# Kernel tuning notes

Measured on AMD Instinct MI355X. Metric: run time of the kernel, lower is better.

## Reference

```python
import jax, jax.numpy as jnp
import numpy as np

N_NODES = 50000
N_EDGES = 800000
D = 128
D_OUT = 128


def setup_inputs() -> dict:
    key = jax.random.key(0)
    k1, k2, k3, k4, k5 = jax.random.split(key, 5)
    feature = jax.random.normal(k1, (N_NODES, D), dtype=jnp.float32)
    src = jax.random.randint(k2, (N_EDGES,), 0, N_NODES)
    dst = jax.random.randint(k3, (N_EDGES,), 0, N_NODES)
    W = jax.random.normal(k4, (D_OUT, 2 * D), dtype=jnp.float32) * (1.0 / np.sqrt(2 * D))
    b = jax.random.normal(k5, (D_OUT,), dtype=jnp.float32) * 0.01
    return {"feature": feature, "src": src, "dst": dst, "W": W, "b": b}


def reference(feature, src, dst, W, b):
    # copy_src: message m_e = feature[src_e]; mean reduce over incoming edges per dst node
    msgs = feature[src]                                             # [E, D] gather
    agg = jax.ops.segment_sum(msgs, dst, num_segments=N_NODES)      # [N, D]
    deg = jax.ops.segment_sum(jnp.ones((N_EDGES,), jnp.float32), dst,
                              num_segments=N_NODES)                 # [N]
    h = agg / jnp.maximum(deg, 1.0)[:, None]                        # mean; 0-degree nodes stay 0
    x = jnp.concatenate([h, feature], axis=1)                       # [N, 2D]
    return x @ W.T + b                                              # [N, D_OUT]
```

## Files before the change

### kernel.cpp

```cpp
#include <hip/hip_runtime.h>
#include <hip/hip_bf16.h>


#define D_IN 128
#define NB 391
#define BSHIFT 7
#define EPB 4096
#define CAPMAX 2680

typedef __attribute__((ext_vector_type(8))) short bf16x8;
typedef __attribute__((ext_vector_type(4))) float f32x4;

static __device__ inline unsigned short f2bf(float x) {
    union { float f; unsigned u; } c; c.f = x;
    unsigned u = c.u;
    unsigned r = u + 0x7FFFu + ((u >> 16) & 1u);
    return (unsigned short)(r >> 16);
}
static __device__ inline float bflo(unsigned u) { return __uint_as_float(u << 16); }
static __device__ inline float bfhi(unsigned u) { return __uint_as_float(u & 0xFFFF0000u); }

__global__ __launch_bounds__(256) void convert_kernel(const float* __restrict__ feat,
                                                      const float* __restrict__ W,
                                                      unsigned short* __restrict__ X,
                                                      unsigned short* __restrict__ Wbf,
                                                      int* __restrict__ bcursor,
                                                      int M, int blocks_f, int CAP) {
    int b = blockIdx.x;
    if (b < blocks_f) {
        size_t idx = ((size_t)b * 256 + threadIdx.x) * 8;
        if (idx >= (size_t)M * 128) return;
        int row = (int)(idx >> 7);
        int col = (int)(idx & 127);
        float4 v0 = *reinterpret_cast<const float4*>(feat + idx);
        float4 v1 = *reinterpret_cast<const float4*>(feat + idx + 4);
        uint4 p;
        p.x = (unsigned)f2bf(v0.x) | ((unsigned)f2bf(v0.y) << 16);
        p.y = (unsigned)f2bf(v0.z) | ((unsigned)f2bf(v0.w) << 16);
        p.z = (unsigned)f2bf(v1.x) | ((unsigned)f2bf(v1.y) << 16);
        p.w = (unsigned)f2bf(v1.z) | ((unsigned)f2bf(v1.w) << 16);
        *reinterpret_cast<uint4*>(X + (size_t)row * 256 + 128 + col) = p;
    } else if (b < blocks_f + 16) {
        int idx = ((b - blocks_f) * 256 + (int)threadIdx.x) * 8;
        if (idx >= 128 * 256) return;
        float4 v0 = *reinterpret_cast<const float4*>(W + idx);
        float4 v1 = *reinterpret_cast<const float4*>(W + idx + 4);
        uint4 p;
        p.x = (unsigned)f2bf(v0.x) | ((unsigned)f2bf(v0.y) << 16);
        p.y = (unsigned)f2bf(v0.z) | ((unsigned)f2bf(v0.w) << 16);
        p.z = (unsigned)f2bf(v1.x) | ((unsigned)f2bf(v1.y) << 16);
        p.w = (unsigned)f2bf(v1.z) | ((unsigned)f2bf(v1.w) << 16);
        *reinterpret_cast<uint4*>(Wbf + idx) = p;
    } else {
        for (int i = threadIdx.x; i < NB; i += 256) bcursor[i] = i * CAP;
    }
}

__global__ __launch_bounds__(256) void coarse_scatter_kernel(
    const int* __restrict__ src, const int* __restrict__ dst,
    int* __restrict__ bcursor, unsigned* __restrict__ bedges,
    int CAP, int nE) {
    __shared__ int hist[NB];
    __shared__ int lofs[NB + 1];
    __shared__ int rnk[NB];
    __shared__ int gbase[NB];
    __shared__ int wsum[4];
    __shared__ unsigned staged[EPB];

    const int tid = threadIdx.x;
    const int e0 = blockIdx.x * EPB;
    for (int i = tid; i < NB; i += 256) { hist[i] = 0; rnk[i] = 0; }
    __syncthreads();

    for (int k = 0; k < EPB; k += 256) {
        int e = e0 + k + tid;
        if (e < nE) atomicAdd(&hist[dst[e] >> BSHIFT], 1);
    }
    __syncthreads();

    {
        int a = (2 * tid < NB) ? hist[2 * tid] : 0;
        int c = (2 * tid + 1 < NB) ? hist[2 * tid + 1] : 0;
        int ps = a + c;
        int x = ps;
        int lane = tid & 63, wv = tid >> 6;
#pragma unroll
        for (int off = 1; off < 64; off <<= 1) {
            int y = __shfl_up(x, off);
            if (lane >= off) x += y;
        }
        if (lane == 63) wsum[wv] = x;
        __syncthreads();
        if (tid == 0) {
            int s = 0;
#pragma unroll
            for (int w = 0; w < 4; w++) { int v = wsum[w]; wsum[w] = s; s += v; }
        }
        __syncthreads();
        int excl = x - ps + wsum[wv];
        if (2 * tid < NB + 1) lofs[2 * tid] = excl;
        if (2 * tid + 1 < NB + 1) lofs[2 * tid + 1] = excl + a;
    }
    __syncthreads();

    for (int i = tid; i < NB; i += 256)
        if (hist[i] > 0) gbase[i] = atomicAdd(&bcursor[i], hist[i]);

    for (int k = 0; k < EPB; k += 256) {
        int e = e0 + k + tid;
        if (e < nE) {
            int d = dst[e];
            int bk = d >> BSHIFT;
            unsigned ed = ((unsigned)d << 16) | (unsigned)src[e];
            int r = atomicAdd(&rnk[bk], 1);
            staged[lofs[bk] + r] = ed;
        }
    }
    __syncthreads();

    int total = lofs[NB];
    for (int i = tid; i < total; i += 256) {
        unsigned ed = staged[i];
        int bk = (int)(ed >> 23);
        int addr = gbase[bk] + (i - lofs[bk]);
        if (addr < (bk + 1) * CAP) bedges[addr] = ed;
    }
}

__global__ __launch_bounds__(256) void fine_sort_kernel(
    unsigned* __restrict__ bedges, const int* __restrict__ bcursor,
    unsigned* __restrict__ rstart, int CAP, int N) {
    __shared__ int h[128];
    __shared__ int lofs[129];
    __shared__ int rnk[128];
    __shared__ unsigned staged[CAPMAX + 8];

    const int b = blockIdx.x;
    const int S = b * CAP;
    const int tid = threadIdx.x;
    int cnt = min(bcursor[b] - S, CAP);

    if (tid < 128) { h[tid] = 0; rnk[tid] = 0; }
    __syncthreads();
    for (int i = tid; i < cnt; i += 256) {
        unsigned ed = bedges[S + i];
        atomicAdd(&h[(ed >> 16) & 127], 1);
    }
    __syncthreads();
    if (tid < 64) {
        int a = h[2 * tid], c = h[2 * tid + 1];
        int ps = a + c;
        int x = ps;
#pragma unroll
        for (int off = 1; off < 64; off <<= 1) {
            int y = __shfl_up(x, off);
            if (tid >= off) x += y;
        }
        int excl = x - ps;
        lofs[2 * tid] = excl;
        lofs[2 * tid + 1] = excl + a;
        if (tid == 63) lofs[128] = x;
    }
    __syncthreads();
    for (int i = tid; i < cnt; i += 256) {
        unsigned ed = bedges[S + i];
        int ld = (ed >> 16) & 127;
        int r = atomicAdd(&rnk[ld], 1);
        staged[lofs[ld] + r] = ed;
    }
    __syncthreads();
    for (int i = tid; i < cnt; i += 256) bedges[S + i] = staged[i];
    if (tid < 128) {
        int node = b * 128 + tid;
        if (node < N)
            rstart[node] = (((unsigned)(S + lofs[tid])) << 12) | (unsigned)h[tid];
    }
}

__global__ __launch_bounds__(256) void node_agg_kernel(unsigned short* __restrict__ X,
                                                       const unsigned* __restrict__ bedges,
                                                       const unsigned* __restrict__ rstart, int N) {
    int wid = (int)((blockIdx.x * (size_t)blockDim.x + threadIdx.x) >> 6);
    if (wid >= N) return;
    const int lane = threadIdx.x & 63;
    const int q = lane >> 4;
    const int sl = lane & 15;
    const unsigned pk = rstart[wid];
    const int s = (int)(pk >> 12);
    const int cnt = (int)(pk & 4095u);
    const int e = s + cnt;
    const char* Xb = (const char*)X;
    const size_t coff = 256 + (size_t)sl * 16;

    float a0=0.f,a1=0.f,a2=0.f,a3=0.f,a4=0.f,a5=0.f,a6=0.f,a7=0.f;
    int j = s + q;
    for (; j + 4 < e; j += 8) {
        int u0 = (int)(bedges[j] & 0xFFFFu);
        int u1 = (int)(bedges[j + 4] & 0xFFFFu);
        uint4 va = *reinterpret_cast<const uint4*>(Xb + (size_t)u0 * 512 + coff);
        uint4 vb = *reinterpret_cast<const uint4*>(Xb + (size_t)u1 * 512 + coff);
        a0 += bflo(va.x) + bflo(vb.x); a1 += bfhi(va.x) + bfhi(vb.x);
        a2 += bflo(va.y) + bflo(vb.y); a3 += bfhi(va.y) + bfhi(vb.y);
        a4 += bflo(va.z) + bflo(vb.z); a5 += bfhi(va.z) + bfhi(vb.z);
        a6 += bflo(va.w) + bflo(vb.w); a7 += bfhi(va.w) + bfhi(vb.w);
    }
    if (j < e) {
        int u = (int)(bedges[j] & 0xFFFFu);
        uint4 va = *reinterpret_cast<const uint4*>(Xb + (size_t)u * 512 + coff);
        a0 += bflo(va.x); a1 += bfhi(va.x);
        a2 += bflo(va.y); a3 += bfhi(va.y);
        a4 += bflo(va.z); a5 += bfhi(va.z);
        a6 += bflo(va.w); a7 += bfhi(va.w);
    }
    a0 += __shfl_down(a0, 32); a1 += __shfl_down(a1, 32);
    a2 += __shfl_down(a2, 32); a3 += __shfl_down(a3, 32);
    a4 += __shfl_down(a4, 32); a5 += __shfl_down(a5, 32);
    a6 += __shfl_down(a6, 32); a7 += __shfl_down(a7, 32);
    a0 += __shfl_down(a0, 16); a1 += __shfl_down(a1, 16);
    a2 += __shfl_down(a2, 16); a3 += __shfl_down(a3, 16);
    a4 += __shfl_down(a4, 16); a5 += __shfl_down(a5, 16);
    a6 += __shfl_down(a6, 16); a7 += __shfl_down(a7, 16);
    if (lane < 16) {
        float r = 1.0f / fmaxf((float)cnt, 1.0f);
        uint4 p;
        p.x = (unsigned)f2bf(a0 * r) | ((unsigned)f2bf(a1 * r) << 16);
        p.y = (unsigned)f2bf(a2 * r) | ((unsigned)f2bf(a3 * r) << 16);
        p.z = (unsigned)f2bf(a4 * r) | ((unsigned)f2bf(a5 * r) << 16);
        p.w = (unsigned)f2bf(a6 * r) | ((unsigned)f2bf(a7 * r) << 16);
        *reinterpret_cast<uint4*>((char*)X + (size_t)wid * 512 + sl * 16) = p;
    }
}

__global__ __launch_bounds__(256) void gcn_gemm_kernel(
    const unsigned short* __restrict__ X, const unsigned short* __restrict__ Wbf,
    const float* __restrict__ bias, float* __restrict__ out, int M) {

    __shared__ unsigned short A_sh[128 * 128];
    __shared__ unsigned short B_sh[128 * 128];
    char* Ab = (char*)A_sh;
    char* Bb = (char*)B_sh;
    const char* Xb = (const char*)X;
    const char* Wb = (const char*)Wbf;

    const int tid = threadIdx.x;
    const int n0 = blockIdx.x * 128;
    const int wid = tid >> 6;
    const int lane = tid & 63;
    const int wr = wid >> 1;
    const int wc = wid & 1;
    const int fr = lane & 15;
    const int fq = lane >> 4;

    f32x4 acc[4][4];
#pragma unroll
    for (int m = 0; m < 4; m++)
#pragma unroll
        for (int n = 0; n < 4; n++) acc[m][n] = (f32x4)(0.0f);

#pragma unroll
    for (int p = 0; p < 2; p++) {
#pragma unroll
        for (int it = 0; it < 8; it++) {
            int idx = it * 256 + tid;
            int row = idx >> 4;
            int ch = idx & 15;
            int off = ((row << 8) + (ch << 4)) ^ ((row & 7) << 4);
            int nrow = n0 + row;
            uint4 va = make_uint4(0u, 0u, 0u, 0u);
            if (nrow < M)
                va = *reinterpret_cast<const uint4*>(Xb + (size_t)nrow * 512 + p * 256 + ch * 16);
            *reinterpret_cast<uint4*>(Ab + off) = va;
            uint4 vb = *reinterpret_cast<const uint4*>(Wb + (size_t)row * 512 + p * 256 + ch * 16);
            *reinterpret_cast<uint4*>(Bb + off) = vb;
        }
        __syncthreads();

#pragma unroll
        for (int ks = 0; ks < 4; ks++) {
            const int k = ks * 32 + fq * 8;
            bf16x8 af[4], bf_[4];
#pragma unroll
            for (int m = 0; m < 4; m++) {
                int row = wr * 64 + m * 16 + fr;
                int off = ((row << 8) + (k << 1)) ^ ((row & 7) << 4);
                af[m] = *reinterpret_cast<const bf16x8*>(Ab + off);
            }
#pragma unroll
            for (int n = 0; n < 4; n++) {
                int col = wc * 64 + n * 16 + fr;
                int off = ((col << 8) + (k << 1)) ^ ((col & 7) << 4);
                bf_[n] = *reinterpret_cast<const bf16x8*>(Bb + off);
            }
#pragma unroll
            for (int m = 0; m < 4; m++)
#pragma unroll
                for (int n = 0; n < 4; n++)
                    acc[m][n] = __builtin_amdgcn_mfma_f32_16x16x32_bf16(af[m], bf_[n], acc[m][n], 0, 0, 0);
        }
        if (p == 0) __syncthreads();
    }

    float bv[4];
#pragma unroll
    for (int n = 0; n < 4; n++) bv[n] = bias[wc * 64 + n * 16 + fr];

#pragma unroll
    for (int m = 0; m < 4; m++) {
        int rbase = n0 + wr * 64 + m * 16 + fq * 4;
#pragma unroll
        for (int n = 0; n < 4; n++) {
            int col = wc * 64 + n * 16 + fr;
#pragma unroll
            for (int j = 0; j < 4; j++) {
                int r = rbase + j;
                if (r < M) out[(size_t)r * 128 + col] = acc[m][n][j] + bv[n];
            }
        }
    }
}

extern "C" void kernel_launch(void* const* d_in, const int* in_sizes, int n_in,
                              void* d_out, int out_size, void* d_ws, size_t ws_size,
                              hipStream_t stream) {
    const float* feature = (const float*)d_in[0];
    const int*   src     = (const int*)d_in[1];
    const int*   dst     = (const int*)d_in[2];
    const float* W       = (const float*)d_in[3];
    const float* bias    = (const float*)d_in[4];
    float* out = (float*)d_out;

    const int M  = in_sizes[0] / D_IN;
    const int nE = in_sizes[1];

    char* w = (char*)d_ws;
    unsigned short* X   = (unsigned short*)w;
    unsigned short* Wbf = X + (size_t)M * 256;
    int* bcursor = (int*)(Wbf + 128 * 256);
    unsigned* rstart = (unsigned*)(bcursor + NB);
    unsigned* bedges = (unsigned*)(rstart + M);

    size_t fixed = (size_t)((char*)bedges - w);
    long avail = (long)ws_size - (long)fixed;
    int CAP = (int)(avail / (NB * 4));
    if (CAP > CAPMAX) CAP = CAPMAX;
    if (CAP < 1) CAP = 1;

    const int blocks_f = (M * D_IN) / (256 * 8);
    convert_kernel<<<blocks_f + 17, 256, 0, stream>>>(feature, W, X, Wbf, bcursor, M, blocks_f, CAP);
    {
        int blocks = (nE + EPB - 1) / EPB;
        coarse_scatter_kernel<<<blocks, 256, 0, stream>>>(src, dst, bcursor, bedges, CAP, nE);
    }
    {
        int blocks = (M + 127) / 128;
        fine_sort_kernel<<<blocks, 256, 0, stream>>>(bedges, bcursor, rstart, CAP, M);
    }
    {
        size_t totalT = (size_t)M * 64;
        int blocks = (int)((totalT + 255) / 256);
        node_agg_kernel<<<blocks, 256, 0, stream>>>(X, bedges, rstart, M);
    }
    {
        int blocks = (M + 127) / 128;
        gcn_gemm_kernel<<<blocks, 256, 0, stream>>>(X, Wbf, bias, out, M);
    }
}
```

Baseline: 79.87 us.

## Fuse convert with coarse scatter and fine sort with node aggregation

The feature/W conversion and the coarse edge bucketing now run as one kernel, with bucket cursors zeroed by a memset and stored as offsets relative to each bucket. The fine per-bucket sort and the mean aggregation are merged into one 512-thread kernel. It reads the sorted edges straight from LDS, so the sorted-edge write-back and the rstart array are gone. This removes two kernel launches and a global round trip of the edge list. In exchange, aggregation parallelism drops to 8 waves per 128-node bucket, and the gather loop is unrolled to 4 edges per lane.

```diff
diff --git a/kernel.cpp b/kernel.cpp
--- a/kernel.cpp
+++ b/kernel.cpp
@@ -20,15 +20,25 @@
 static __device__ inline float bflo(unsigned u) { return __uint_as_float(u << 16); }
 static __device__ inline float bfhi(unsigned u) { return __uint_as_float(u & 0xFFFF0000u); }
 
-__global__ __launch_bounds__(256) void convert_kernel(const float* __restrict__ feat,
-                                                      const float* __restrict__ W,
-                                                      unsigned short* __restrict__ X,
-                                                      unsigned short* __restrict__ Wbf,
-                                                      int* __restrict__ bcursor,
-                                                      int M, int blocks_f, int CAP) {
-    int b = blockIdx.x;
+__global__ __launch_bounds__(256) void prep_kernel(
+    const float* __restrict__ feat, const float* __restrict__ W,
+    const int* __restrict__ src, const int* __restrict__ dst,
+    unsigned short* __restrict__ X, unsigned short* __restrict__ Wbf,
+    int* __restrict__ bcursor, unsigned* __restrict__ bedges,
+    int M, int nE, int blocks_f, int CAP) {
+
+    __shared__ int hist[NB];
+    __shared__ int lofs[NB + 1];
+    __shared__ int rnk[NB];
+    __shared__ int gbase[NB];
+    __shared__ int wsum[4];
+    __shared__ unsigned staged[EPB];
+
+    const int b = blockIdx.x;
+    const int tid = threadIdx.x;
+
     if (b < blocks_f) {
-        size_t idx = ((size_t)b * 256 + threadIdx.x) * 8;
+        size_t idx = ((size_t)b * 256 + tid) * 8;
         if (idx >= (size_t)M * 128) return;
         int row = (int)(idx >> 7);
         int col = (int)(idx & 127);
@@ -40,8 +50,10 @@
         p.z = (unsigned)f2bf(v1.x) | ((unsigned)f2bf(v1.y) << 16);
         p.w = (unsigned)f2bf(v1.z) | ((unsigned)f2bf(v1.w) << 16);
         *reinterpret_cast<uint4*>(X + (size_t)row * 256 + 128 + col) = p;
-    } else if (b < blocks_f + 16) {
-        int idx = ((b - blocks_f) * 256 + (int)threadIdx.x) * 8;
+        return;
+    }
+    if (b < blocks_f + 16) {
+        int idx = ((b - blocks_f) * 256 + tid) * 8;
         if (idx >= 128 * 256) return;
         float4 v0 = *reinterpret_cast<const float4*>(W + idx);
         float4 v1 = *reinterpret_cast<const float4*>(W + idx + 4);
@@ -51,24 +63,10 @@
         p.z = (unsigned)f2bf(v1.x) | ((unsigned)f2bf(v1.y) << 16);
         p.w = (unsigned)f2bf(v1.z) | ((unsigned)f2bf(v1.w) << 16);
         *reinterpret_cast<uint4*>(Wbf + idx) = p;
-    } else {
-        for (int i = threadIdx.x; i < NB; i += 256) bcursor[i] = i * CAP;
-    }
-}
-
-__global__ __launch_bounds__(256) void coarse_scatter_kernel(
-    const int* __restrict__ src, const int* __restrict__ dst,
-    int* __restrict__ bcursor, unsigned* __restrict__ bedges,
-    int CAP, int nE) {
-    __shared__ int hist[NB];
-    __shared__ int lofs[NB + 1];
-    __shared__ int rnk[NB];
-    __shared__ int gbase[NB];
-    __shared__ int wsum[4];
-    __shared__ unsigned staged[EPB];
-
-    const int tid = threadIdx.x;
-    const int e0 = blockIdx.x * EPB;
+        return;
+    }
+
+    const int e0 = (b - blocks_f - 16) * EPB;
     for (int i = tid; i < NB; i += 256) { hist[i] = 0; rnk[i] = 0; }
     __syncthreads();
 
@@ -104,7 +102,7 @@
     __syncthreads();
 
     for (int i = tid; i < NB; i += 256)
-        if (hist[i] > 0) gbase[i] = atomicAdd(&bcursor[i], hist[i]);
+        if (hist[i] > 0) gbase[i] = i * CAP + atomicAdd(&bcursor[i], hist[i]);
 
     for (int k = 0; k < EPB; k += 256) {
         int e = e0 + k + tid;
@@ -127,9 +125,10 @@
     }
 }
 
-__global__ __launch_bounds__(256) void fine_sort_kernel(
-    unsigned* __restrict__ bedges, const int* __restrict__ bcursor,
-    unsigned* __restrict__ rstart, int CAP, int N) {
+__global__ __launch_bounds__(512) void sort_agg_kernel(
+    unsigned short* __restrict__ X, const unsigned* __restrict__ bedges,
+    const int* __restrict__ bcursor, int CAP, int N) {
+
     __shared__ int h[128];
     __shared__ int lofs[129];
     __shared__ int rnk[128];
@@ -138,11 +137,11 @@
     const int b = blockIdx.x;
     const int S = b * CAP;
     const int tid = threadIdx.x;
-    int cnt = min(bcursor[b] - S, CAP);
+    const int cnt = min(bcursor[b], CAP);
 
     if (tid < 128) { h[tid] = 0; rnk[tid] = 0; }
     __syncthreads();
-    for (int i = tid; i < cnt; i += 256) {
+    for (int i = tid; i < cnt; i += 512) {
         unsigned ed = bedges[S + i];
         atomicAdd(&h[(ed >> 16) & 127], 1);
     }
@@ -162,72 +161,74 @@
         if (tid == 63) lofs[128] = x;
     }
     __syncthreads();
-    for (int i = tid; i < cnt; i += 256) {
+    for (int i = tid; i < cnt; i += 512) {
         unsigned ed = bedges[S + i];
         int ld = (ed >> 16) & 127;
         int r = atomicAdd(&rnk[ld], 1);
         staged[lofs[ld] + r] = ed;
     }
     __syncthreads();
-    for (int i = tid; i < cnt; i += 256) bedges[S + i] = staged[i];
-    if (tid < 128) {
-        int node = b * 128 + tid;
-        if (node < N)
-            rstart[node] = (((unsigned)(S + lofs[tid])) << 12) | (unsigned)h[tid];
-    }
-}
-
-__global__ __launch_bounds__(256) void node_agg_kernel(unsigned short* __restrict__ X,
-                                                       const unsigned* __restrict__ bedges,
-                                                       const unsigned* __restrict__ rstart, int N) {
-    int wid = (int)((blockIdx.x * (size_t)blockDim.x + threadIdx.x) >> 6);
-    if (wid >= N) return;
-    const int lane = threadIdx.x & 63;
+
+    const int w = tid >> 6;
+    const int lane = tid & 63;
     const int q = lane >> 4;
     const int sl = lane & 15;
-    const unsigned pk = rstart[wid];
-    const int s = (int)(pk >> 12);
-    const int cnt = (int)(pk & 4095u);
-    const int e = s + cnt;
     const char* Xb = (const char*)X;
     const size_t coff = 256 + (size_t)sl * 16;
-
-    float a0=0.f,a1=0.f,a2=0.f,a3=0.f,a4=0.f,a5=0.f,a6=0.f,a7=0.f;
-    int j = s + q;
-    for (; j + 4 < e; j += 8) {
-        int u0 = (int)(bedges[j] & 0xFFFFu);
-        int u1 = (int)(bedges[j + 4] & 0xFFFFu);
-        uint4 va = *reinterpret_cast<const uint4*>(Xb + (size_t)u0 * 512 + coff);
-        uint4 vb = *reinterpret_cast<const uint4*>(Xb + (size_t)u1 * 512 + coff);
-        a0 += bflo(va.x) + bflo(vb.x); a1 += bfhi(va.x) + bfhi(vb.x);
-        a2 += bflo(va.y) + bflo(vb.y); a3 += bfhi(va.y) + bfhi(vb.y);
-        a4 += bflo(va.z) + bflo(vb.z); a5 += bfhi(va.z) + bfhi(vb.z);
-        a6 += bflo(va.w) + bflo(vb.w); a7 += bfhi(va.w) + bfhi(vb.w);
-    }
-    if (j < e) {
-        int u = (int)(bedges[j] & 0xFFFFu);
-        uint4 va = *reinterpret_cast<const uint4*>(Xb + (size_t)u * 512 + coff);
-        a0 += bflo(va.x); a1 += bfhi(va.x);
-        a2 += bflo(va.y); a3 += bfhi(va.y);
-        a4 += bflo(va.z); a5 += bfhi(va.z);
-        a6 += bflo(va.w); a7 += bfhi(va.w);
-    }
-    a0 += __shfl_down(a0, 32); a1 += __shfl_down(a1, 32);
-    a2 += __shfl_down(a2, 32); a3 += __shfl_down(a3, 32);
-    a4 += __shfl_down(a4, 32); a5 += __shfl_down(a5, 32);
-    a6 += __shfl_down(a6, 32); a7 += __shfl_down(a7, 32);
-    a0 += __shfl_down(a0, 16); a1 += __shfl_down(a1, 16);
-    a2 += __shfl_down(a2, 16); a3 += __shfl_down(a3, 16);
-    a4 += __shfl_down(a4, 16); a5 += __shfl_down(a5, 16);
-    a6 += __shfl_down(a6, 16); a7 += __shfl_down(a7, 16);
-    if (lane < 16) {
-        float r = 1.0f / fmaxf((float)cnt, 1.0f);
-        uint4 p;
-        p.x = (unsigned)f2bf(a0 * r) | ((unsigned)f2bf(a1 * r) << 16);
-        p.y = (unsigned)f2bf(a2 * r) | ((unsigned)f2bf(a3 * r) << 16);
-        p.z = (unsigned)f2bf(a4 * r) | ((unsigned)f2bf(a5 * r) << 16);
-        p.w = (unsigned)f2bf(a6 * r) | ((unsigned)f2bf(a7 * r) << 16);
-        *reinterpret_cast<uint4*>((char*)X + (size_t)wid * 512 + sl * 16) = p;
+    const int n0 = b * 128;
+
+    for (int ln = w; ln < 128; ln += 8) {
+        int node = n0 + ln;
+        if (node >= N) break;
+        const int s = lofs[ln];
+        const int deg = h[ln];
+        const int e = s + deg;
+
+        float a0=0.f,a1=0.f,a2=0.f,a3=0.f,a4=0.f,a5=0.f,a6=0.f,a7=0.f;
+        int j = s + q;
+        for (; j + 12 < e; j += 16) {
+            int u0 = (int)(staged[j] & 0xFFFFu);
+            int u1 = (int)(staged[j + 4] & 0xFFFFu);
+            int u2 = (int)(staged[j + 8] & 0xFFFFu);
+            int u3 = (int)(staged[j + 12] & 0xFFFFu);
+            uint4 va = *reinterpret_cast<const uint4*>(Xb + (size_t)u0 * 512 + coff);
+            uint4 vb = *reinterpret_cast<const uint4*>(Xb + (size_t)u1 * 512 + coff);
+            uint4 vc = *reinterpret_cast<const uint4*>(Xb + (size_t)u2 * 512 + coff);
+            uint4 vd = *reinterpret_cast<const uint4*>(Xb + (size_t)u3 * 512 + coff);
+            a0 += (bflo(va.x) + bflo(vb.x)) + (bflo(vc.x) + bflo(vd.x));
+            a1 += (bfhi(va.x) + bfhi(vb.x)) + (bfhi(vc.x) + bfhi(vd.x));
+            a2 += (bflo(va.y) + bflo(vb.y)) + (bflo(vc.y) + bflo(vd.y));
+            a3 += (bfhi(va.y) + bfhi(vb.y)) + (bfhi(vc.y) + bfhi(vd.y));
+            a4 += (bflo(va.z) + bflo(vb.z)) + (bflo(vc.z) + bflo(vd.z));
+            a5 += (bfhi(va.z) + bfhi(vb.z)) + (bfhi(vc.z) + bfhi(vd.z));
+            a6 += (bflo(va.w) + bflo(vb.w)) + (bflo(vc.w) + bflo(vd.w));
+            a7 += (bfhi(va.w) + bfhi(vb.w)) + (bfhi(vc.w) + bfhi(vd.w));
+        }
+        for (; j < e; j += 4) {
+            int u = (int)(staged[j] & 0xFFFFu);
+            uint4 va = *reinterpret_cast<const uint4*>(Xb + (size_t)u * 512 + coff);
+            a0 += bflo(va.x); a1 += bfhi(va.x);
+            a2 += bflo(va.y); a3 += bfhi(va.y);
+            a4 += bflo(va.z); a5 += bfhi(va.z);
+            a6 += bflo(va.w); a7 += bfhi(va.w);
+        }
+        a0 += __shfl_down(a0, 32); a1 += __shfl_down(a1, 32);
+        a2 += __shfl_down(a2, 32); a3 += __shfl_down(a3, 32);
+        a4 += __shfl_down(a4, 32); a5 += __shfl_down(a5, 32);
+        a6 += __shfl_down(a6, 32); a7 += __shfl_down(a7, 32);
+        a0 += __shfl_down(a0, 16); a1 += __shfl_down(a1, 16);
+        a2 += __shfl_down(a2, 16); a3 += __shfl_down(a3, 16);
+        a4 += __shfl_down(a4, 16); a5 += __shfl_down(a5, 16);
+        a6 += __shfl_down(a6, 16); a7 += __shfl_down(a7, 16);
+        if (lane < 16) {
+            float r = 1.0f / fmaxf((float)deg, 1.0f);
+            uint4 p;
+            p.x = (unsigned)f2bf(a0 * r) | ((unsigned)f2bf(a1 * r) << 16);
+            p.y = (unsigned)f2bf(a2 * r) | ((unsigned)f2bf(a3 * r) << 16);
+            p.z = (unsigned)f2bf(a4 * r) | ((unsigned)f2bf(a5 * r) << 16);
+            p.w = (unsigned)f2bf(a6 * r) | ((unsigned)f2bf(a7 * r) << 16);
+            *reinterpret_cast<uint4*>((char*)X + (size_t)node * 512 + sl * 16) = p;
+        }
     }
 }
 
@@ -336,8 +337,7 @@
     unsigned short* X   = (unsigned short*)w;
     unsigned short* Wbf = X + (size_t)M * 256;
     int* bcursor = (int*)(Wbf + 128 * 256);
-    unsigned* rstart = (unsigned*)(bcursor + NB);
-    unsigned* bedges = (unsigned*)(rstart + M);
+    unsigned* bedges = (unsigned*)(bcursor + NB);
 
     size_t fixed = (size_t)((char*)bedges - w);
     long avail = (long)ws_size - (long)fixed;
@@ -345,20 +345,16 @@
     if (CAP > CAPMAX) CAP = CAPMAX;
     if (CAP < 1) CAP = 1;
 
+    hipMemsetAsync(bcursor, 0, NB * sizeof(int), stream);
+
     const int blocks_f = (M * D_IN) / (256 * 8);
-    convert_kernel<<<blocks_f + 17, 256, 0, stream>>>(feature, W, X, Wbf, bcursor, M, blocks_f, CAP);
-    {
-        int blocks = (nE + EPB - 1) / EPB;
-        coarse_scatter_kernel<<<blocks, 256, 0, stream>>>(src, dst, bcursor, bedges, CAP, nE);
-    }
+    const int blocks_c = (nE + EPB - 1) / EPB;
+    prep_kernel<<<blocks_f + 16 + blocks_c, 256, 0, stream>>>(
+        feature, W, src, dst, X, Wbf, bcursor, bedges, M, nE, blocks_f, CAP);
+
     {
         int blocks = (M + 127) / 128;
-        fine_sort_kernel<<<blocks, 256, 0, stream>>>(bedges, bcursor, rstart, CAP, M);
-    }
-    {
-        size_t totalT = (size_t)M * 64;
-        int blocks = (int)((totalT + 255) / 256);
-        node_agg_kernel<<<blocks, 256, 0, stream>>>(X, bedges, rstart, M);
+        sort_agg_kernel<<<blocks, 512, 0, stream>>>(X, bedges, bcursor, CAP, M);
     }
     {
         int blocks = (M + 127) / 128;
```

After: 87.55 us. 9.6% more time.

## Fuse conversion and coarse edge scatter into one prep kernel; unroll gather by four

Applied to the files above, without the earlier changes.

Merges the feature/weight bf16 conversion and the coarse bucket scatter into a single launch by giving them disjoint block ranges. The bucket cursor initialisation becomes a memset, and cursors are now relative offsets, with the bucket base added at use. This removes one kernel launch and lets the conversion and the scatter overlap. Separately, the node aggregation gather loop is unrolled from two to four outstanding row loads per lane to expose more memory-level parallelism. The cost is higher register use and shared memory allocated even for conversion blocks, which may reduce occupancy.

```diff
diff --git a/kernel.cpp b/kernel.cpp
--- a/kernel.cpp
+++ b/kernel.cpp
@@ -20,15 +20,25 @@
 static __device__ inline float bflo(unsigned u) { return __uint_as_float(u << 16); }
 static __device__ inline float bfhi(unsigned u) { return __uint_as_float(u & 0xFFFF0000u); }
 
-__global__ __launch_bounds__(256) void convert_kernel(const float* __restrict__ feat,
-                                                      const float* __restrict__ W,
-                                                      unsigned short* __restrict__ X,
-                                                      unsigned short* __restrict__ Wbf,
-                                                      int* __restrict__ bcursor,
-                                                      int M, int blocks_f, int CAP) {
-    int b = blockIdx.x;
+__global__ __launch_bounds__(256) void prep_kernel(
+    const float* __restrict__ feat, const float* __restrict__ W,
+    const int* __restrict__ src, const int* __restrict__ dst,
+    unsigned short* __restrict__ X, unsigned short* __restrict__ Wbf,
+    int* __restrict__ bcursor, unsigned* __restrict__ bedges,
+    int M, int nE, int blocks_f, int CAP) {
+
+    __shared__ int hist[NB];
+    __shared__ int lofs[NB + 1];
+    __shared__ int rnk[NB];
+    __shared__ int gbase[NB];
+    __shared__ int wsum[4];
+    __shared__ unsigned staged[EPB];
+
+    const int b = blockIdx.x;
+    const int tid = threadIdx.x;
+
     if (b < blocks_f) {
-        size_t idx = ((size_t)b * 256 + threadIdx.x) * 8;
+        size_t idx = ((size_t)b * 256 + tid) * 8;
         if (idx >= (size_t)M * 128) return;
         int row = (int)(idx >> 7);
         int col = (int)(idx & 127);
@@ -40,8 +50,10 @@
         p.z = (unsigned)f2bf(v1.x) | ((unsigned)f2bf(v1.y) << 16);
         p.w = (unsigned)f2bf(v1.z) | ((unsigned)f2bf(v1.w) << 16);
         *reinterpret_cast<uint4*>(X + (size_t)row * 256 + 128 + col) = p;
-    } else if (b < blocks_f + 16) {
-        int idx = ((b - blocks_f) * 256 + (int)threadIdx.x) * 8;
+        return;
+    }
+    if (b < blocks_f + 16) {
+        int idx = ((b - blocks_f) * 256 + tid) * 8;
         if (idx >= 128 * 256) return;
         float4 v0 = *reinterpret_cast<const float4*>(W + idx);
         float4 v1 = *reinterpret_cast<const float4*>(W + idx + 4);
@@ -51,24 +63,10 @@
         p.z = (unsigned)f2bf(v1.x) | ((unsigned)f2bf(v1.y) << 16);
         p.w = (unsigned)f2bf(v1.z) | ((unsigned)f2bf(v1.w) << 16);
         *reinterpret_cast<uint4*>(Wbf + idx) = p;
-    } else {
-        for (int i = threadIdx.x; i < NB; i += 256) bcursor[i] = i * CAP;
-    }
-}
-
-__global__ __launch_bounds__(256) void coarse_scatter_kernel(
-    const int* __restrict__ src, const int* __restrict__ dst,
-    int* __restrict__ bcursor, unsigned* __restrict__ bedges,
-    int CAP, int nE) {
-    __shared__ int hist[NB];
-    __shared__ int lofs[NB + 1];
-    __shared__ int rnk[NB];
-    __shared__ int gbase[NB];
-    __shared__ int wsum[4];
-    __shared__ unsigned staged[EPB];
-
-    const int tid = threadIdx.x;
-    const int e0 = blockIdx.x * EPB;
+        return;
+    }
+
+    const int e0 = (b - blocks_f - 16) * EPB;
     for (int i = tid; i < NB; i += 256) { hist[i] = 0; rnk[i] = 0; }
     __syncthreads();
 
@@ -104,7 +102,7 @@
     __syncthreads();
 
     for (int i = tid; i < NB; i += 256)
-        if (hist[i] > 0) gbase[i] = atomicAdd(&bcursor[i], hist[i]);
+        if (hist[i] > 0) gbase[i] = i * CAP + atomicAdd(&bcursor[i], hist[i]);
 
     for (int k = 0; k < EPB; k += 256) {
         int e = e0 + k + tid;
@@ -138,7 +136,7 @@
     const int b = blockIdx.x;
     const int S = b * CAP;
     const int tid = threadIdx.x;
-    int cnt = min(bcursor[b] - S, CAP);
+    int cnt = min(bcursor[b], CAP);
 
     if (tid < 128) { h[tid] = 0; rnk[tid] = 0; }
     __syncthreads();
@@ -194,17 +192,25 @@
 
     float a0=0.f,a1=0.f,a2=0.f,a3=0.f,a4=0.f,a5=0.f,a6=0.f,a7=0.f;
     int j = s + q;
-    for (; j + 4 < e; j += 8) {
+    for (; j + 12 < e; j += 16) {
         int u0 = (int)(bedges[j] & 0xFFFFu);
         int u1 = (int)(bedges[j + 4] & 0xFFFFu);
+        int u2 = (int)(bedges[j + 8] & 0xFFFFu);
+        int u3 = (int)(bedges[j + 12] & 0xFFFFu);
         uint4 va = *reinterpret_cast<const uint4*>(Xb + (size_t)u0 * 512 + coff);
         uint4 vb = *reinterpret_cast<const uint4*>(Xb + (size_t)u1 * 512 + coff);
-        a0 += bflo(va.x) + bflo(vb.x); a1 += bfhi(va.x) + bfhi(vb.x);
-        a2 += bflo(va.y) + bflo(vb.y); a3 += bfhi(va.y) + bfhi(vb.y);
-        a4 += bflo(va.z) + bflo(vb.z); a5 += bfhi(va.z) + bfhi(vb.z);
-        a6 += bflo(va.w) + bflo(vb.w); a7 += bfhi(va.w) + bfhi(vb.w);
-    }
-    if (j < e) {
+        uint4 vc = *reinterpret_cast<const uint4*>(Xb + (size_t)u2 * 512 + coff);
+        uint4 vd = *reinterpret_cast<const uint4*>(Xb + (size_t)u3 * 512 + coff);
+        a0 += (bflo(va.x) + bflo(vb.x)) + (bflo(vc.x) + bflo(vd.x));
+        a1 += (bfhi(va.x) + bfhi(vb.x)) + (bfhi(vc.x) + bfhi(vd.x));
+        a2 += (bflo(va.y) + bflo(vb.y)) + (bflo(vc.y) + bflo(vd.y));
+        a3 += (bfhi(va.y) + bfhi(vb.y)) + (bfhi(vc.y) + bfhi(vd.y));
+        a4 += (bflo(va.z) + bflo(vb.z)) + (bflo(vc.z) + bflo(vd.z));
+        a5 += (bfhi(va.z) + bfhi(vb.z)) + (bfhi(vc.z) + bfhi(vd.z));
+        a6 += (bflo(va.w) + bflo(vb.w)) + (bflo(vc.w) + bflo(vd.w));
+        a7 += (bfhi(va.w) + bfhi(vb.w)) + (bfhi(vc.w) + bfhi(vd.w));
+    }
+    for (; j < e; j += 4) {
         int u = (int)(bedges[j] & 0xFFFFu);
         uint4 va = *reinterpret_cast<const uint4*>(Xb + (size_t)u * 512 + coff);
         a0 += bflo(va.x); a1 += bfhi(va.x);
@@ -345,12 +351,13 @@
     if (CAP > CAPMAX) CAP = CAPMAX;
     if (CAP < 1) CAP = 1;
 
+    hipMemsetAsync(bcursor, 0, NB * sizeof(int), stream);
+
     const int blocks_f = (M * D_IN) / (256 * 8);
-    convert_kernel<<<blocks_f + 17, 256, 0, stream>>>(feature, W, X, Wbf, bcursor, M, blocks_f, CAP);
-    {
-        int blocks = (nE + EPB - 1) / EPB;
-        coarse_scatter_kernel<<<blocks, 256, 0, stream>>>(src, dst, bcursor, bedges, CAP, nE);
-    }
+    const int blocks_c = (nE + EPB - 1) / EPB;
+    prep_kernel<<<blocks_f + 16 + blocks_c, 256, 0, stream>>>(
+        feature, W, src, dst, X, Wbf, bcursor, bedges, M, nE, blocks_f, CAP);
+
     {
         int blocks = (M + 127) / 128;
         fine_sort_kernel<<<blocks, 256, 0, stream>>>(bedges, bcursor, rstart, CAP, M);
```

Result: slower. 84.64 us (+6.0%).

## Gather neighbor features from an FP8 copy and split X into separate buffers

Applied to the files above, without the earlier changes.

The convert kernel now also writes an FP8 (e4m3) copy of the features. The aggregation kernel gathers 8 bytes per lane from this copy instead of 16 bytes of bf16, which halves the random-gather traffic, and its loop is unrolled to four edges per iteration. The combined X buffer is split into separate Xh and Xf arrays that the GEMM reads from. The bucket cursor init moves to a memset, with the bucket base offset added inside the scatter and sort kernels. FP8 accumulation loses precision in the mean aggregation, which risks tolerance failures.

```diff
diff --git a/kernel.cpp b/kernel.cpp
--- a/kernel.cpp
+++ b/kernel.cpp
@@ -10,6 +10,7 @@
 
 typedef __attribute__((ext_vector_type(8))) short bf16x8;
 typedef __attribute__((ext_vector_type(4))) float f32x4;
+typedef __attribute__((ext_vector_type(2))) float f32x2;
 
 static __device__ inline unsigned short f2bf(float x) {
     union { float f; unsigned u; } c; c.f = x;
@@ -17,21 +18,17 @@
     unsigned r = u + 0x7FFFu + ((u >> 16) & 1u);
     return (unsigned short)(r >> 16);
 }
-static __device__ inline float bflo(unsigned u) { return __uint_as_float(u << 16); }
-static __device__ inline float bfhi(unsigned u) { return __uint_as_float(u & 0xFFFF0000u); }
 
 __global__ __launch_bounds__(256) void convert_kernel(const float* __restrict__ feat,
                                                       const float* __restrict__ W,
-                                                      unsigned short* __restrict__ X,
+                                                      unsigned short* __restrict__ Xf,
+                                                      unsigned char* __restrict__ Xq,
                                                       unsigned short* __restrict__ Wbf,
-                                                      int* __restrict__ bcursor,
-                                                      int M, int blocks_f, int CAP) {
+                                                      int M, int blocks_f) {
     int b = blockIdx.x;
     if (b < blocks_f) {
         size_t idx = ((size_t)b * 256 + threadIdx.x) * 8;
         if (idx >= (size_t)M * 128) return;
-        int row = (int)(idx >> 7);
-        int col = (int)(idx & 127);
         float4 v0 = *reinterpret_cast<const float4*>(feat + idx);
         float4 v1 = *reinterpret_cast<const float4*>(feat + idx + 4);
         uint4 p;
@@ -39,8 +36,13 @@
         p.y = (unsigned)f2bf(v0.z) | ((unsigned)f2bf(v0.w) << 16);
         p.z = (unsigned)f2bf(v1.x) | ((unsigned)f2bf(v1.y) << 16);
         p.w = (unsigned)f2bf(v1.z) | ((unsigned)f2bf(v1.w) << 16);
-        *reinterpret_cast<uint4*>(X + (size_t)row * 256 + 128 + col) = p;
-    } else if (b < blocks_f + 16) {
+        *reinterpret_cast<uint4*>(Xf + idx) = p;
+        int w0 = __builtin_amdgcn_cvt_pk_fp8_f32(v0.x, v0.y, 0, false);
+        w0 = __builtin_amdgcn_cvt_pk_fp8_f32(v0.z, v0.w, w0, true);
+        int w1 = __builtin_amdgcn_cvt_pk_fp8_f32(v1.x, v1.y, 0, false);
+        w1 = __builtin_amdgcn_cvt_pk_fp8_f32(v1.z, v1.w, w1, true);
+        *reinterpret_cast<uint2*>(Xq + idx) = make_uint2((unsigned)w0, (unsigned)w1);
+    } else {
         int idx = ((b - blocks_f) * 256 + (int)threadIdx.x) * 8;
         if (idx >= 128 * 256) return;
         float4 v0 = *reinterpret_cast<const float4*>(W + idx);
@@ -51,8 +53,6 @@
         p.z = (unsigned)f2bf(v1.x) | ((unsigned)f2bf(v1.y) << 16);
         p.w = (unsigned)f2bf(v1.z) | ((unsigned)f2bf(v1.w) << 16);
         *reinterpret_cast<uint4*>(Wbf + idx) = p;
-    } else {
-        for (int i = threadIdx.x; i < NB; i += 256) bcursor[i] = i * CAP;
     }
 }
 
@@ -104,7 +104,7 @@
     __syncthreads();
 
     for (int i = tid; i < NB; i += 256)
-        if (hist[i] > 0) gbase[i] = atomicAdd(&bcursor[i], hist[i]);
+        if (hist[i] > 0) gbase[i] = i * CAP + atomicAdd(&bcursor[i], hist[i]);
 
     for (int k = 0; k < EPB; k += 256) {
         int e = e0 + k + tid;
@@ -138,7 +138,7 @@
     const int b = blockIdx.x;
     const int S = b * CAP;
     const int tid = threadIdx.x;
-    int cnt = min(bcursor[b] - S, CAP);
+    int cnt = min(bcursor[b], CAP);
 
     if (tid < 128) { h[tid] = 0; rnk[tid] = 0; }
     __syncthreads();
@@ -177,7 +177,18 @@
     }
 }
 
-__global__ __launch_bounds__(256) void node_agg_kernel(unsigned short* __restrict__ X,
+static __device__ inline void acc8(uint2 v, float& a0, float& a1, float& a2, float& a3,
+                                   float& a4, float& a5, float& a6, float& a7) {
+    f32x2 p0 = __builtin_amdgcn_cvt_pk_f32_fp8((int)v.x, false);
+    f32x2 p1 = __builtin_amdgcn_cvt_pk_f32_fp8((int)v.x, true);
+    f32x2 p2 = __builtin_amdgcn_cvt_pk_f32_fp8((int)v.y, false);
+    f32x2 p3 = __builtin_amdgcn_cvt_pk_f32_fp8((int)v.y, true);
+    a0 += p0.x; a1 += p0.y; a2 += p1.x; a3 += p1.y;
+    a4 += p2.x; a5 += p2.y; a6 += p3.x; a7 += p3.y;
+}
+
+__global__ __launch_bounds__(256) void node_agg_kernel(const unsigned char* __restrict__ Xq,
+                                                       unsigned short* __restrict__ Xh,
                                                        const unsigned* __restrict__ bedges,
                                                        const unsigned* __restrict__ rstart, int N) {
     int wid = (int)((blockIdx.x * (size_t)blockDim.x + threadIdx.x) >> 6);
@@ -189,28 +200,28 @@
     const int s = (int)(pk >> 12);
     const int cnt = (int)(pk & 4095u);
     const int e = s + cnt;
-    const char* Xb = (const char*)X;
-    const size_t coff = 256 + (size_t)sl * 16;
+    const size_t coff = (size_t)sl * 8;
 
     float a0=0.f,a1=0.f,a2=0.f,a3=0.f,a4=0.f,a5=0.f,a6=0.f,a7=0.f;
     int j = s + q;
-    for (; j + 4 < e; j += 8) {
+    for (; j + 12 < e; j += 16) {
         int u0 = (int)(bedges[j] & 0xFFFFu);
         int u1 = (int)(bedges[j + 4] & 0xFFFFu);
-        uint4 va = *reinterpret_cast<const uint4*>(Xb + (size_t)u0 * 512 + coff);
-        uint4 vb = *reinterpret_cast<const uint4*>(Xb + (size_t)u1 * 512 + coff);
-        a0 += bflo(va.x) + bflo(vb.x); a1 += bfhi(va.x) + bfhi(vb.x);
-        a2 += bflo(va.y) + bflo(vb.y); a3 += bfhi(va.y) + bfhi(vb.y);
-        a4 += bflo(va.z) + bflo(vb.z); a5 += bfhi(va.z) + bfhi(vb.z);
-        a6 += bflo(va.w) + bflo(vb.w); a7 += bfhi(va.w) + bfhi(vb.w);
-    }
-    if (j < e) {
+        int u2 = (int)(bedges[j + 8] & 0xFFFFu);
+        int u3 = (int)(bedges[j + 12] & 0xFFFFu);
+        uint2 va = *reinterpret_cast<const uint2*>(Xq + (size_t)u0 * 128 + coff);
+        uint2 vb = *reinterpret_cast<const uint2*>(Xq + (size_t)u1 * 128 + coff);
+        uint2 vc = *reinterpret_cast<const uint2*>(Xq + (size_t)u2 * 128 + coff);
+        uint2 vd = *reinterpret_cast<const uint2*>(Xq + (size_t)u3 * 128 + coff);
+        acc8(va, a0,a1,a2,a3,a4,a5,a6,a7);
+        acc8(vb, a0,a1,a2,a3,a4,a5,a6,a7);
+        acc8(vc, a0,a1,a2,a3,a4,a5,a6,a7);
+        acc8(vd, a0,a1,a2,a3,a4,a5,a6,a7);
+    }
+    for (; j < e; j += 4) {
         int u = (int)(bedges[j] & 0xFFFFu);
-        uint4 va = *reinterpret_cast<const uint4*>(Xb + (size_t)u * 512 + coff);
-        a0 += bflo(va.x); a1 += bfhi(va.x);
-        a2 += bflo(va.y); a3 += bfhi(va.y);
-        a4 += bflo(va.z); a5 += bfhi(va.z);
-        a6 += bflo(va.w); a7 += bfhi(va.w);
+        uint2 va = *reinterpret_cast<const uint2*>(Xq + (size_t)u * 128 + coff);
+        acc8(va, a0,a1,a2,a3,a4,a5,a6,a7);
     }
     a0 += __shfl_down(a0, 32); a1 += __shfl_down(a1, 32);
     a2 += __shfl_down(a2, 32); a3 += __shfl_down(a3, 32);
@@ -227,19 +238,19 @@
         p.y = (unsigned)f2bf(a2 * r) | ((unsigned)f2bf(a3 * r) << 16);
         p.z = (unsigned)f2bf(a4 * r) | ((unsigned)f2bf(a5 * r) << 16);
         p.w = (unsigned)f2bf(a6 * r) | ((unsigned)f2bf(a7 * r) << 16);
-        *reinterpret_cast<uint4*>((char*)X + (size_t)wid * 512 + sl * 16) = p;
+        *reinterpret_cast<uint4*>((char*)Xh + (size_t)wid * 256 + sl * 16) = p;
     }
 }
 
 __global__ __launch_bounds__(256) void gcn_gemm_kernel(
-    const unsigned short* __restrict__ X, const unsigned short* __restrict__ Wbf,
+    const unsigned short* __restrict__ Xh, const unsigned short* __restrict__ Xf,
+    const unsigned short* __restrict__ Wbf,
     const float* __restrict__ bias, float* __restrict__ out, int M) {
 
     __shared__ unsigned short A_sh[128 * 128];
     __shared__ unsigned short B_sh[128 * 128];
     char* Ab = (char*)A_sh;
     char* Bb = (char*)B_sh;
-    const char* Xb = (const char*)X;
     const char* Wb = (const char*)Wbf;
 
     const int tid = threadIdx.x;
@@ -259,6 +270,7 @@
 
 #pragma unroll
     for (int p = 0; p < 2; p++) {
+        const char* Asrc = (const char*)(p == 0 ? Xh : Xf);
 #pragma unroll
         for (int it = 0; it < 8; it++) {
             int idx = it * 256 + tid;
@@ -268,7 +280,7 @@
             int nrow = n0 + row;
             uint4 va = make_uint4(0u, 0u, 0u, 0u);
             if (nrow < M)
-                va = *reinterpret_cast<const uint4*>(Xb + (size_t)nrow * 512 + p * 256 + ch * 16);
+                va = *reinterpret_cast<const uint4*>(Asrc + (size_t)nrow * 256 + ch * 16);
             *reinterpret_cast<uint4*>(Ab + off) = va;
             uint4 vb = *reinterpret_cast<const uint4*>(Wb + (size_t)row * 512 + p * 256 + ch * 16);
             *reinterpret_cast<uint4*>(Bb + off) = vb;
@@ -333,8 +345,10 @@
     const int nE = in_sizes[1];
 
     char* w = (char*)d_ws;
-    unsigned short* X   = (unsigned short*)w;
-    unsigned short* Wbf = X + (size_t)M * 256;
+    unsigned short* Xh  = (unsigned short*)w;
+    unsigned short* Xf  = Xh + (size_t)M * 128;
+    unsigned char*  Xq  = (unsigned char*)(Xf + (size_t)M * 128);
+    unsigned short* Wbf = (unsigned short*)(Xq + (size_t)M * 128);
     int* bcursor = (int*)(Wbf + 128 * 256);
     unsigned* rstart = (unsigned*)(bcursor + NB);
     unsigned* bedges = (unsigned*)(rstart + M);
@@ -345,8 +359,10 @@
     if (CAP > CAPMAX) CAP = CAPMAX;
     if (CAP < 1) CAP = 1;
 
+    hipMemsetAsync(bcursor, 0, NB * sizeof(int), stream);
+
     const int blocks_f = (M * D_IN) / (256 * 8);
-    convert_kernel<<<blocks_f + 17, 256, 0, stream>>>(feature, W, X, Wbf, bcursor, M, blocks_f, CAP);
+    convert_kernel<<<blocks_f + 16, 256, 0, stream>>>(feature, W, Xf, Xq, Wbf, M, blocks_f);
     {
         int blocks = (nE + EPB - 1) / EPB;
         coarse_scatter_kernel<<<blocks, 256, 0, stream>>>(src, dst, bcursor, bedges, CAP, nE);
@@ -358,10 +374,10 @@
     {
         size_t totalT = (size_t)M * 64;
         int blocks = (int)((totalT + 255) / 256);
-        node_agg_kernel<<<blocks, 256, 0, stream>>>(X, bedges, rstart, M);
+        node_agg_kernel<<<blocks, 256, 0, stream>>>(Xq, Xh, bedges, rstart, M);
     }
     {
         int blocks = (M + 127) / 128;
-        gcn_gemm_kernel<<<blocks, 256, 0, stream>>>(X, Wbf, bias, out, M);
-    }
-}
+        gcn_gemm_kernel<<<blocks, 256, 0, stream>>>(Xh, Xf, Wbf, bias, out, M);
+    }
+}
```

Result: slower. 83.58 us (+4.6%).
